# Kernel tuning notes

Measured on AMD Instinct MI355X. Metric: run time of the kernel, lower is better.

Reference implementation:

```python
import jax, jax.numpy as jnp
import numpy as np

EMBED = 1024
HEADS = 16


def setup_inputs() -> dict:
    key = jax.random.key(0)
    ks = jax.random.split(key, 12)
    s = 1.0 / np.sqrt(EMBED)
    return {
        "x": jax.random.normal(ks[0], (1, EMBED, 128, 128), jnp.float32),
        "masks": jax.random.normal(ks[1], (200, 128, 128), jnp.float32),
        "Wq": jax.random.normal(ks[2], (EMBED, EMBED), jnp.float32) * s,
        "bq": jax.random.normal(ks[3], (EMBED,), jnp.float32) * 0.02,
        "Wk": jax.random.normal(ks[4], (EMBED, EMBED), jnp.float32) * s,
        "bk": jax.random.normal(ks[5], (EMBED,), jnp.float32) * 0.02,
        "Wv": jax.random.normal(ks[6], (EMBED, EMBED), jnp.float32) * s,
        "bv": jax.random.normal(ks[7], (EMBED,), jnp.float32) * 0.02,
        "Wc": jax.random.normal(ks[8], (EMBED, EMBED), jnp.float32) * s,
        "bc": jax.random.normal(ks[9], (EMBED,), jnp.float32) * 0.02,
    }


def reference(x, masks, Wq, bq, Wk, bk, Wv, bv, Wc, bc):
    # x: [1, C, H, W], masks: [Q, H, W]  (way4 branch, batch must be 1)
    N, C, H, W = x.shape
    Q = masks.shape[0]
    HW = H * W
    nh = HEADS
    hd = C // nh

    xs = x.reshape(C, HW).T                      # [HW, C] pixel tokens
    m = jax.nn.sigmoid(masks).reshape(Q, HW).T   # [HW, Q]

    # mask-weighted mean pooling (avoid materializing [HW, Q, C])
    w = jnp.sum(m, axis=0)                       # [Q]
    mean = jnp.einsum('lq,lc->qc', m, xs) / (w[:, None] + 0.001)  # [Q, C]

    seq = jnp.concatenate([mean, xs], axis=0)    # [L, C], L = Q + HW
    L = Q + HW

    q = (mean @ Wq.T + bq).reshape(Q, nh, hd) * (hd ** -0.5)
    k = (seq @ Wk.T + bk).reshape(L, nh, hd)
    v = (seq @ Wv.T + bv).reshape(L, nh, hd)

    # bool attn mask [Q, L]: True = disallowed
    qq = ~jnp.eye(Q, dtype=bool)                 # only self among pooled queries
    qp = (m.T <= 0.9)                            # pixels with sigmoid <= 0.9 masked
    attn_mask = jnp.concatenate([qq, qp], axis=1)  # [Q, L]

    scores = jnp.einsum('qhd,lhd->hql', q, k)    # [nh, Q, L]
    scores = jnp.where(attn_mask[None], -jnp.inf, scores)
    probs = jax.nn.softmax(scores, axis=-1)
    ctx = jnp.einsum('hql,lhd->qhd', probs, v).reshape(Q, C)
    out = ctx @ Wc.T + bc                        # [Q, out_dim]
    return out.reshape(Q, 1, -1)                 # match torch [Q, batch=1, out_dim]
```

## Files before the change

kernel.cpp:

```cpp
#include <hip/hip_runtime.h>
#include <math.h>

#define HW_  16384
#define Q_   200
#define C_   1024
#define L_   16584
#define NH_  16
#define HD_  64
#define CAP  512
#define KSPLIT 8
#define KCH  (HW_ / KSPLIT)
#define ASPLIT 4
#define SK   4

typedef __attribute__((ext_vector_type(8))) __bf16 bf16x8;
typedef __attribute__((ext_vector_type(8))) unsigned short u16x8;
typedef __attribute__((ext_vector_type(4))) unsigned short u16x4;
typedef __attribute__((ext_vector_type(4))) float f32x4;

__device__ inline unsigned short f2bf(float f) {
  unsigned int u = __float_as_uint(f);
  u += 0x7fff + ((u >> 16) & 1);
  return (unsigned short)(u >> 16);
}
__device__ inline float bf2f(unsigned short u) {
  return __uint_as_float((unsigned int)u << 16);
}


__global__ __launch_bounds__(256) void k_sig_compact(const float* __restrict__ masks,
                                                     unsigned short* __restrict__ msigbf,
                                                     float* __restrict__ w,
                                                     int* __restrict__ cnt,
                                                     int* __restrict__ idxg) {
  int q = blockIdx.x;
  int tid = threadIdx.x;
  unsigned short* obf = msigbf + (size_t)q * HW_;
  if (q >= Q_) {
    u16x4 z = {0, 0, 0, 0};
    for (int i = tid; i < HW_ / 4; i += 256) *(u16x4*)&obf[i * 4] = z;
    return;
  }
  const float* mrow = masks + (size_t)q * HW_;
  const int base = tid * 64;
  unsigned long long bits = 0;
  float s = 0.f;
  #pragma unroll
  for (int j4 = 0; j4 < 16; j4++) {
    float4 v = *(const float4*)&mrow[base + j4 * 4];
    float sg0 = 1.f / (1.f + expf(-v.x));
    float sg1 = 1.f / (1.f + expf(-v.y));
    float sg2 = 1.f / (1.f + expf(-v.z));
    float sg3 = 1.f / (1.f + expf(-v.w));
    u16x4 o = {f2bf(sg0), f2bf(sg1), f2bf(sg2), f2bf(sg3)};
    *(u16x4*)&obf[base + j4 * 4] = o;
    s += sg0 + sg1 + sg2 + sg3;
    if (sg0 > 0.9f) bits |= 1ull << (j4 * 4 + 0);
    if (sg1 > 0.9f) bits |= 1ull << (j4 * 4 + 1);
    if (sg2 > 0.9f) bits |= 1ull << (j4 * 4 + 2);
    if (sg3 > 0.9f) bits |= 1ull << (j4 * 4 + 3);
  }
  int my = __popcll(bits);

  __shared__ float red[256];
  __shared__ int sc[256];
  red[tid] = s;
  sc[tid] = my;
  __syncthreads();
  for (int off = 128; off > 0; off >>= 1) {
    if (tid < off) red[tid] += red[tid + off];
    __syncthreads();
  }
  if (tid == 0) w[q] = red[0];
  for (int off = 1; off < 256; off <<= 1) {
    int v = sc[tid];
    int add = (tid >= off) ? sc[tid - off] : 0;
    __syncthreads();
    sc[tid] = v + add;
    __syncthreads();
  }
  int excl = sc[tid] - my;
  int total = sc[255];
  int* orow = idxg + (size_t)q * CAP;
  int off = 1 + excl;
  for (int j = 0; j < 64; j++) {
    if ((bits >> j) & 1ull) {
      if (off < CAP) orow[off] = Q_ + base + j;
      off++;
    }
  }
  if (tid == 0) {
    orow[0] = q;
    int c = 1 + total;
    cnt[q] = c < CAP ? c : CAP;
  }
}

__global__ __launch_bounds__(256) void k_xcast(const float* __restrict__ x,
                                               unsigned short* __restrict__ xbf,
                                               unsigned short* __restrict__ seqbf) {
  __shared__ float t[32][33];
  int l0 = blockIdx.x * 32, c0 = blockIdx.y * 32;
  int tx = threadIdx.x, ty = threadIdx.y;
  #pragma unroll
  for (int i = 0; i < 32; i += 8) {
    float v = x[(size_t)(c0 + ty + i) * HW_ + l0 + tx];
    t[ty + i][tx] = v;
    xbf[(size_t)(c0 + ty + i) * HW_ + l0 + tx] = f2bf(v);
  }
  __syncthreads();
  #pragma unroll
  for (int i = 0; i < 32; i += 8)
    seqbf[(size_t)(Q_ + l0 + ty + i) * C_ + c0 + tx] = f2bf(t[tx][ty + i]);
}

__global__ __launch_bounds__(256) void k_cast4(const float* __restrict__ s0,
                                               const float* __restrict__ s1,
                                               const float* __restrict__ s2,
                                               const float* __restrict__ s3,
                                               unsigned short* __restrict__ d0,
                                               unsigned short* __restrict__ d1,
                                               unsigned short* __restrict__ d2,
                                               unsigned short* __restrict__ d3) {
  const float* src = (blockIdx.y == 0) ? s0 : (blockIdx.y == 1) ? s1
                     : (blockIdx.y == 2) ? s2 : s3;
  unsigned short* dst = (blockIdx.y == 0) ? d0 : (blockIdx.y == 1) ? d1
                        : (blockIdx.y == 2) ? d2 : d3;
  int i = (blockIdx.x * 256 + threadIdx.x) * 4;
  float4 v = *(const float4*)&src[i];
  u16x4 o = {f2bf(v.x), f2bf(v.y), f2bf(v.z), f2bf(v.w)};
  *(u16x4*)&dst[i] = o;
}

#define GBM 128
#define GBN 128
#define GBK 32

__global__ __launch_bounds__(512) void k_gemm_kv(const unsigned short* __restrict__ A,
                                                 const unsigned short* __restrict__ Bk,
                                                 const unsigned short* __restrict__ Bv,
                                                 const float* __restrict__ bk,
                                                 const float* __restrict__ bv,
                                                 unsigned short* __restrict__ Ko,
                                                 unsigned short* __restrict__ Vo,
                                                 int M, int K) {
  __shared__ __attribute__((aligned(16))) unsigned short smem[3][3 * GBM * GBK];
  int w = blockIdx.x;
  int nbm = gridDim.x >> 3;
  int t = (w >> 3) + (w & 7) * nbm;
  int bm = (t >> 3) * GBM;
  int bn = (t & 7) * GBN;
  int tid = threadIdx.x;
  int wid = tid >> 6, lane = tid & 63;
  int w2 = wid & 3;
  int wr = w2 >> 1, wc = w2 & 1;
  int fq = lane >> 4, fr = lane & 15;
  int srow = lane >> 2;
  int scol = (((lane & 3) ^ ((lane >> 3) & 3)) * 8);
  int sslot = (fq ^ ((fr >> 1) & 3)) * 8;
  int boff = (wid < 4) ? GBM * GBK : 2 * GBM * GBK;

  auto stage = [&](int buf, int k0) {
    #pragma unroll
    for (int i = 0; i < 3; i++) {
      int ci = wid * 3 + i;
      const unsigned short* src;
      if (ci < 8) {
        int gA = bm + ci * 16 + srow; if (gA > M - 1) gA = M - 1;
        src = A + (size_t)gA * K + k0 + scol;
      } else if (ci < 16) {
        src = Bk + (size_t)(bn + (ci - 8) * 16 + srow) * K + k0 + scol;
      } else {
        src = Bv + (size_t)(bn + (ci - 16) * 16 + srow) * K + k0 + scol;
      }
      __builtin_amdgcn_global_load_lds(
          (const __attribute__((address_space(1))) void*)src,
          (__attribute__((address_space(3))) void*)((char*)&smem[buf][0] + ci * 1024),
          16, 0, 0);
    }
  };

  f32x4 acc[4][4] = {};
  const int NT = K / GBK;
  stage(0, 0);
  stage(1, GBK);
  for (int it = 0; it < NT; it++) {
    int cur = it % 3;
    asm volatile("" ::: "memory");
    __builtin_amdgcn_s_barrier();
    asm volatile("" ::: "memory");
    if (it + 2 < NT) {
      stage((it + 2) % 3, (it + 2) * GBK);
      asm volatile("s_waitcnt vmcnt(6)" ::: "memory");
    } else if (it + 1 < NT) {
      asm volatile("s_waitcnt vmcnt(3)" ::: "memory");
    } else {
      asm volatile("s_waitcnt vmcnt(0)" ::: "memory");
    }
    const unsigned short (*As)[GBK]  = (const unsigned short (*)[GBK])(&smem[cur][0]);
    const unsigned short (*Bts)[GBK] = (const unsigned short (*)[GBK])(&smem[cur][0] + boff);
    bf16x8 af[4], bfr[4];
    #pragma unroll
    for (int mi = 0; mi < 4; mi++)
      af[mi] = *(const bf16x8*)&As[wr * 64 + mi * 16 + fr][sslot];
    #pragma unroll
    for (int ni = 0; ni < 4; ni++)
      bfr[ni] = *(const bf16x8*)&Bts[wc * 64 + ni * 16 + fr][sslot];
    __builtin_amdgcn_s_setprio(1);
    #pragma unroll
    for (int mi = 0; mi < 4; mi++)
      #pragma unroll
      for (int ni = 0; ni < 4; ni++)
        acc[mi][ni] = __builtin_amdgcn_mfma_f32_16x16x32_bf16(bfr[ni], af[mi], acc[mi][ni], 0, 0, 0);
    __builtin_amdgcn_s_setprio(0);
  }
  const float* bias = (wid < 4) ? bk : bv;
  unsigned short* Cout = (wid < 4) ? Ko : Vo;
  #pragma unroll
  for (int mi = 0; mi < 4; mi++) {
    int m = bm + wr * 64 + mi * 16 + fr;
    if (m >= M) continue;
    #pragma unroll
    for (int ni = 0; ni < 4; ni++) {
      int n0 = bn + wc * 64 + ni * 16 + fq * 4;
      float4 b4 = *(const float4*)&bias[n0];
      u16x4 o = {f2bf(acc[mi][ni][0] + b4.x), f2bf(acc[mi][ni][1] + b4.y),
                 f2bf(acc[mi][ni][2] + b4.z), f2bf(acc[mi][ni][3] + b4.w)};
      *(u16x4*)&Cout[(size_t)m * C_ + n0] = o;
    }
  }
}

__global__ __launch_bounds__(256) void k_gemm_meank(const unsigned short* __restrict__ A,
                                                    const unsigned short* __restrict__ B,
                                                    float* __restrict__ partial) {
  __shared__ __attribute__((aligned(16))) unsigned short As[2][GBM][GBK];
  __shared__ __attribute__((aligned(16))) unsigned short Bs[2][GBN][GBK];
  int bm = blockIdx.y * GBM, bn = blockIdx.x * GBN;
  int kc = blockIdx.z;
  int tid = threadIdx.x;
  int wid = tid >> 6, lane = tid & 63;
  int wr = wid >> 1, wc = wid & 1;
  int fq = lane >> 4, fr = lane & 15;
  int srow = lane >> 2;
  int scol = (((lane & 3) ^ ((lane >> 3) & 3)) * 8);
  int sslot = (fq ^ ((fr >> 1) & 3)) * 8;

  auto stage = [&](int buf, int k0) {
    #pragma unroll
    for (int i = 0; i < 2; i++) {
      int r = wid * 32 + i * 16 + srow;
      __builtin_amdgcn_global_load_lds(
          (const __attribute__((address_space(1))) void*)(A + (size_t)(bm + r) * HW_ + k0 + scol),
          (__attribute__((address_space(3))) void*)((char*)&As[buf][0][0] + (wid * 2 + i) * 1024),
          16, 0, 0);
      __builtin_amdgcn_global_load_lds(
          (const __attribute__((address_space(1))) void*)(B + (size_t)(bn + r) * HW_ + k0 + scol),
          (__attribute__((address_space(3))) void*)((char*)&Bs[buf][0][0] + (wid * 2 + i) * 1024),
          16, 0, 0);
    }
  };

  f32x4 acc[4][4] = {};
  int kbeg = kc * KCH;
  const int NT = KCH / GBK;
  stage(0, kbeg);
  __syncthreads();
  int cur = 0;
  for (int it = 0; it < NT; it++) {
    if (it + 1 < NT) stage(cur ^ 1, kbeg + (it + 1) * GBK);
    bf16x8 af[4], bfr[4];
    #pragma unroll
    for (int mi = 0; mi < 4; mi++)
      af[mi] = *(const bf16x8*)&As[cur][wr * 64 + mi * 16 + fr][sslot];
    #pragma unroll
    for (int ni = 0; ni < 4; ni++)
      bfr[ni] = *(const bf16x8*)&Bs[cur][wc * 64 + ni * 16 + fr][sslot];
    #pragma unroll
    for (int mi = 0; mi < 4; mi++)
      #pragma unroll
      for (int ni = 0; ni < 4; ni++)
        acc[mi][ni] = __builtin_amdgcn_mfma_f32_16x16x32_bf16(bfr[ni], af[mi], acc[mi][ni], 0, 0, 0);
    __syncthreads();
    cur ^= 1;
  }
  #pragma unroll
  for (int mi = 0; mi < 4; mi++) {
    int m = bm + wr * 64 + mi * 16 + fr;
    #pragma unroll
    for (int ni = 0; ni < 4; ni++) {
      int n0 = bn + wc * 64 + ni * 16 + fq * 4;
      *(f32x4*)&partial[((size_t)kc * 256 + m) * C_ + n0] = acc[mi][ni];
    }
  }
}

__global__ __launch_bounds__(256) void k_mean_reduce(const float* __restrict__ partial,
                                                     const float* __restrict__ w,
                                                     unsigned short* __restrict__ seqbf) {
  int m = blockIdx.x;
  float rs = 1.f / (w[m] + 0.001f);
  for (int n = threadIdx.x; n < C_; n += 256) {
    float s = 0.f;
    #pragma unroll
    for (int kc = 0; kc < KSPLIT; kc++)
      s += partial[((size_t)kc * 256 + m) * C_ + n];
    seqbf[(size_t)m * C_ + n] = f2bf(s * rs);
  }
}

__global__ __launch_bounds__(256) void k_gemm_splitk_bf(const unsigned short* __restrict__ A,
                                                        const unsigned short* __restrict__ B,
                                                        float* __restrict__ partial,
                                                        int M, int K) {
  __shared__ __attribute__((aligned(16))) unsigned short As[2][GBM][GBK];
  __shared__ __attribute__((aligned(16))) unsigned short Bs[2][GBN][GBK];
  int bm = blockIdx.y * GBM, bn = blockIdx.x * GBN;
  int kc = blockIdx.z;
  int kchunk = K / SK;
  int tid = threadIdx.x;
  int wid = tid >> 6, lane = tid & 63;
  int wr = wid >> 1, wc = wid & 1;
  int fq = lane >> 4, fr = lane & 15;
  int srow = lane >> 2;
  int scol = (((lane & 3) ^ ((lane >> 3) & 3)) * 8);
  int sslot = (fq ^ ((fr >> 1) & 3)) * 8;

  auto stage = [&](int buf, int k0) {
    #pragma unroll
    for (int i = 0; i < 2; i++) {
      int r = wid * 32 + i * 16 + srow;
      int gA = bm + r; if (gA > M - 1) gA = M - 1;
      __builtin_amdgcn_global_load_lds(
          (const __attribute__((address_space(1))) void*)(A + (size_t)gA * K + k0 + scol),
          (__attribute__((address_space(3))) void*)((char*)&As[buf][0][0] + (wid * 2 + i) * 1024),
          16, 0, 0);
      __builtin_amdgcn_global_load_lds(
          (const __attribute__((address_space(1))) void*)(B + (size_t)(bn + r) * K + k0 + scol),
          (__attribute__((address_space(3))) void*)((char*)&Bs[buf][0][0] + (wid * 2 + i) * 1024),
          16, 0, 0);
    }
  };

  f32x4 acc[4][4] = {};
  int kbeg = kc * kchunk;
  const int NT = kchunk / GBK;
  stage(0, kbeg);
  __syncthreads();
  int cur = 0;
  for (int it = 0; it < NT; it++) {
    if (it + 1 < NT) stage(cur ^ 1, kbeg + (it + 1) * GBK);
    bf16x8 af[4], bfr[4];
    #pragma unroll
    for (int mi = 0; mi < 4; mi++)
      af[mi] = *(const bf16x8*)&As[cur][wr * 64 + mi * 16 + fr][sslot];
    #pragma unroll
    for (int ni = 0; ni < 4; ni++)
      bfr[ni] = *(const bf16x8*)&Bs[cur][wc * 64 + ni * 16 + fr][sslot];
    #pragma unroll
    for (int mi = 0; mi < 4; mi++)
      #pragma unroll
      for (int ni = 0; ni < 4; ni++)
        acc[mi][ni] = __builtin_amdgcn_mfma_f32_16x16x32_bf16(bfr[ni], af[mi], acc[mi][ni], 0, 0, 0);
    __syncthreads();
    cur ^= 1;
  }
  #pragma unroll
  for (int mi = 0; mi < 4; mi++) {
    int m = bm + wr * 64 + mi * 16 + fr;
    #pragma unroll
    for (int ni = 0; ni < 4; ni++) {
      int n0 = bn + wc * 64 + ni * 16 + fq * 4;
      *(f32x4*)&partial[((size_t)kc * 256 + m) * C_ + n0] = acc[mi][ni];
    }
  }
}

__global__ __launch_bounds__(256) void k_splitk_reduce(const float* __restrict__ partial,
                                                       const float* __restrict__ bias,
                                                       float* __restrict__ outf) {
  int m = blockIdx.x;
  for (int n = threadIdx.x; n < C_; n += 256) {
    float s = 0.f;
    #pragma unroll
    for (int kc = 0; kc < SK; kc++)
      s += partial[((size_t)kc * 256 + m) * C_ + n];
    outf[(size_t)m * C_ + n] = s + bias[n];
  }
}

__global__ __launch_bounds__(256) void k_attn_split(const float* __restrict__ qpart,
                                                    const float* __restrict__ bq,
                                                    const unsigned short* __restrict__ kb,
                                                    const unsigned short* __restrict__ vb,
                                                    const int* __restrict__ cnt_g,
                                                    const int* __restrict__ idxg,
                                                    float* __restrict__ pmax,
                                                    float* __restrict__ psum,
                                                    float* __restrict__ pacc) {
  int q = blockIdx.x, h = blockIdx.y, sp = blockIdx.z;
  int tid = threadIdx.x;
  int lane = tid & 63, wid = tid >> 6;

  __shared__ float qs[64];
  __shared__ float sc[CAP / ASPLIT];
  __shared__ int   ls[CAP / ASPLIT];
  __shared__ float wred[4];
  __shared__ float accb[4][64];

  int cnt = cnt_g[q];
  int cq = (cnt + ASPLIT - 1) / ASPLIT;
  int beg = sp * cq;
  int end = beg + cq; if (end > cnt) end = cnt;
  int ns = end - beg; if (ns < 0) ns = 0;

  if (tid < 64) {
    float s = bq[h * HD_ + tid];
    #pragma unroll
    for (int kc = 0; kc < SK; kc++)
      s += qpart[((size_t)kc * 256 + q) * C_ + h * HD_ + tid];
    qs[tid] = s * 0.125f;
  }
  __syncthreads();

  for (int i0 = 0; i0 < ns; i0 += 64) {
    int i = i0 + (tid >> 2);
    if (i < ns) {
      int sub = tid & 3;
      int l = idxg[(size_t)q * CAP + beg + i];
      const u16x8* kr = (const u16x8*)(kb + (size_t)l * C_ + h * HD_ + sub * 16);
      u16x8 kv0 = kr[0], kv1 = kr[1];
      float s = 0.f;
      #pragma unroll
      for (int e = 0; e < 8; e++) s = fmaf(qs[sub * 16 + e], bf2f(kv0[e]), s);
      #pragma unroll
      for (int e = 0; e < 8; e++) s = fmaf(qs[sub * 16 + 8 + e], bf2f(kv1[e]), s);
      s += __shfl_xor(s, 1);
      s += __shfl_xor(s, 2);
      if (sub == 0) { sc[i] = s; ls[i] = l; }
    }
  }
  __syncthreads();

  float lm = (tid < ns) ? sc[tid] : -INFINITY;
  #pragma unroll
  for (int off = 32; off; off >>= 1) lm = fmaxf(lm, __shfl_xor(lm, off));
  if (lane == 0) wred[wid] = lm;
  __syncthreads();
  float m4 = fmaxf(fmaxf(wred[0], wred[1]), fmaxf(wred[2], wred[3]));

  float e = 0.f;
  if (tid < ns) {
    e = expf(sc[tid] - m4);
    sc[tid] = e;
  }
  float lsum = e;
  #pragma unroll
  for (int off = 32; off; off >>= 1) lsum += __shfl_xor(lsum, off);
  __syncthreads();
  if (lane == 0) wred[wid] = lsum;
  __syncthreads();
  float S4 = wred[0] + wred[1] + wred[2] + wred[3];

  float acc = 0.f;
  for (int j = wid; j < ns; j += 4)
    acc = fmaf(sc[j], bf2f(vb[(size_t)ls[j] * C_ + h * HD_ + lane]), acc);
  accb[wid][lane] = acc;
  __syncthreads();

  int pidx = (q * NH_ + h) * ASPLIT + sp;
  if (tid < 64)
    pacc[(size_t)pidx * 64 + tid] =
        accb[0][tid] + accb[1][tid] + accb[2][tid] + accb[3][tid];
  if (tid == 0) {
    pmax[pidx] = (ns > 0) ? m4 : -INFINITY;
    psum[pidx] = S4;
  }
}

__global__ __launch_bounds__(64) void k_attn_merge(const float* __restrict__ pmax,
                                                   const float* __restrict__ psum,
                                                   const float* __restrict__ pacc,
                                                   unsigned short* __restrict__ ctxbf) {
  int q = blockIdx.x, h = blockIdx.y;
  int d = threadIdx.x;
  int base = (q * NH_ + h) * ASPLIT;
  float M = -INFINITY;
  #pragma unroll
  for (int s = 0; s < ASPLIT; s++) M = fmaxf(M, pmax[base + s]);
  float S = 0.f, a = 0.f;
  #pragma unroll
  for (int s = 0; s < ASPLIT; s++) {
    float wgt = expf(pmax[base + s] - M);
    S += psum[base + s] * wgt;
    a += pacc[(size_t)(base + s) * 64 + d] * wgt;
  }
  ctxbf[(size_t)q * C_ + h * HD_ + d] = f2bf(a / S);
}

extern "C" void kernel_launch(void* const* d_in, const int* in_sizes, int n_in,
                              void* d_out, int out_size, void* d_ws, size_t ws_size,
                              hipStream_t stream) {
  const float* x     = (const float*)d_in[0];
  const float* masks = (const float*)d_in[1];
  const float* Wq    = (const float*)d_in[2];
  const float* bq    = (const float*)d_in[3];
  const float* Wk    = (const float*)d_in[4];
  const float* bk    = (const float*)d_in[5];
  const float* Wv    = (const float*)d_in[6];
  const float* bv    = (const float*)d_in[7];
  const float* Wc    = (const float*)d_in[8];
  const float* bc    = (const float*)d_in[9];
  float* out = (float*)d_out;

  char* p = (char*)d_ws;
  auto alloc = [&](size_t bytes) {
    char* r = p;
    p += (bytes + 255) & ~(size_t)255;
    return r;
  };
  float* w       = (float*)alloc(1024);
  float* partial = (float*)alloc((size_t)KSPLIT * 256 * C_ * 4);
  float* qpart   = (float*)alloc((size_t)SK * 256 * C_ * 4);
  int*   cnt     = (int*)alloc(1024);
  int*   idxg    = (int*)alloc((size_t)Q_ * CAP * 4);
  float* pmax    = (float*)alloc((size_t)Q_ * NH_ * ASPLIT * 4);
  float* psum    = (float*)alloc((size_t)Q_ * NH_ * ASPLIT * 4);
  float* pacc    = (float*)alloc((size_t)Q_ * NH_ * ASPLIT * 64 * 4);
  unsigned short* msigbf = (unsigned short*)alloc((size_t)256 * HW_ * 2);
  unsigned short* xbf    = (unsigned short*)alloc((size_t)C_ * HW_ * 2);
  unsigned short* seqbf  = (unsigned short*)alloc((size_t)L_ * C_ * 2);
  unsigned short* wkbf   = (unsigned short*)alloc((size_t)C_ * C_ * 2);
  unsigned short* wvbf   = (unsigned short*)alloc((size_t)C_ * C_ * 2);
  unsigned short* wqbf   = (unsigned short*)alloc((size_t)C_ * C_ * 2);
  unsigned short* wcbf   = (unsigned short*)alloc((size_t)C_ * C_ * 2);
  unsigned short* ctxbf  = (unsigned short*)alloc((size_t)256 * C_ * 2);
  unsigned short* kbuf   = (unsigned short*)alloc((size_t)L_ * C_ * 2);
  unsigned short* vbuf   = (unsigned short*)alloc((size_t)L_ * C_ * 2);

  k_sig_compact<<<256, 256, 0, stream>>>(masks, msigbf, w, cnt, idxg);
  k_xcast<<<dim3(HW_ / 32, C_ / 32), dim3(32, 8), 0, stream>>>(x, xbf, seqbf);
  k_cast4<<<dim3(C_ * C_ / 1024, 4), 256, 0, stream>>>(Wk, Wv, Wq, Wc,
                                                       wkbf, wvbf, wqbf, wcbf);
  k_gemm_meank<<<dim3(C_ / GBN, 2, KSPLIT), 256, 0, stream>>>(msigbf, xbf, partial);
  k_mean_reduce<<<Q_, 256, 0, stream>>>(partial, w, seqbf);
  k_gemm_splitk_bf<<<dim3(C_ / GBN, 2, SK), 256, 0, stream>>>(seqbf, wqbf, qpart, Q_, C_);
  k_gemm_kv<<<8 * ((L_ + GBM - 1) / GBM), 512, 0, stream>>>(
      seqbf, wkbf, wvbf, bk, bv, kbuf, vbuf, L_, C_);
  k_attn_split<<<dim3(Q_, NH_, ASPLIT), 256, 0, stream>>>(
      qpart, bq, kbuf, vbuf, cnt, idxg, pmax, psum, pacc);
  k_attn_merge<<<dim3(Q_, NH_), 64, 0, stream>>>(pmax, psum, pacc, ctxbf);
  k_gemm_splitk_bf<<<dim3(C_ / GBN, 2, SK), 256, 0, stream>>>(ctxbf, wcbf, partial, Q_, C_);
  k_splitk_reduce<<<Q_, 256, 0, stream>>>(partial, bc, out);
}
```

Measured before the change: 267.2 us.

## Restructure K/V projection GEMM into 256x128 tiles with concatenated weights and quarter pipelining

Replaces the fused K/V GEMM with a kernel that treats Wk and Wv as one concatenated 2048-row weight matrix, using 256x128 output tiles with BK=64 and double-buffered LDS. The loads are split into A and B halves interleaved with four MFMA quarter-steps, with separate waitcnt/barrier points so global-to-LDS copies overlap compute. The goal is higher arithmetic intensity per tile and better latency hiding in the dominant GEMM. In exchange LDS use and register pressure go up, and the fixed swizzle adds complexity. The hardcoded grid mapping (130 M-tiles) ties the kernel to this problem size.

```diff
diff --git a/kernel.cpp b/kernel.cpp
--- a/kernel.cpp
+++ b/kernel.cpp
@@ -26,7 +26,6 @@
 __device__ inline float bf2f(unsigned short u) {
   return __uint_as_float((unsigned int)u << 16);
 }
-
 
 __global__ __launch_bounds__(256) void k_sig_compact(const float* __restrict__ masks,
                                                      unsigned short* __restrict__ msigbf,
@@ -136,97 +135,138 @@
 #define GBN 128
 #define GBK 32
 
-__global__ __launch_bounds__(512) void k_gemm_kv(const unsigned short* __restrict__ A,
-                                                 const unsigned short* __restrict__ Bk,
-                                                 const unsigned short* __restrict__ Bv,
-                                                 const float* __restrict__ bk,
-                                                 const float* __restrict__ bv,
-                                                 unsigned short* __restrict__ Ko,
-                                                 unsigned short* __restrict__ Vo,
-                                                 int M, int K) {
-  __shared__ __attribute__((aligned(16))) unsigned short smem[3][3 * GBM * GBK];
-  int w = blockIdx.x;
-  int nbm = gridDim.x >> 3;
-  int t = (w >> 3) + (w & 7) * nbm;
-  int bm = (t >> 3) * GBM;
-  int bn = (t & 7) * GBN;
+__global__ __launch_bounds__(512) void k_gemm_kv8(const unsigned short* __restrict__ A,
+                                                  const unsigned short* __restrict__ Wkv,
+                                                  const float* __restrict__ bk,
+                                                  const float* __restrict__ bv,
+                                                  unsigned short* __restrict__ Ko,
+                                                  unsigned short* __restrict__ Vo,
+                                                  int M) {
+  __shared__ __attribute__((aligned(16))) unsigned short lds[2][24576];
+  const int K = 1024;
+  int wg = blockIdx.x;
+  int t = (wg >> 3) + (wg & 7) * 130;
+  int bm = (t >> 4) * 256;
+  int bn = (t & 15) * 128;
   int tid = threadIdx.x;
   int wid = tid >> 6, lane = tid & 63;
-  int w2 = wid & 3;
-  int wr = w2 >> 1, wc = w2 & 1;
+  int wm = wid >> 1;
+  int wn = wid & 1;
   int fq = lane >> 4, fr = lane & 15;
-  int srow = lane >> 2;
-  int scol = (((lane & 3) ^ ((lane >> 3) & 3)) * 8);
-  int sslot = (fq ^ ((fr >> 1) & 3)) * 8;
-  int boff = (wid < 4) ? GBM * GBK : 2 * GBM * GBK;
-
-  auto stage = [&](int buf, int k0) {
-    #pragma unroll
-    for (int i = 0; i < 3; i++) {
-      int ci = wid * 3 + i;
-      const unsigned short* src;
-      if (ci < 8) {
-        int gA = bm + ci * 16 + srow; if (gA > M - 1) gA = M - 1;
-        src = A + (size_t)gA * K + k0 + scol;
-      } else if (ci < 16) {
-        src = Bk + (size_t)(bn + (ci - 8) * 16 + srow) * K + k0 + scol;
-      } else {
-        src = Bv + (size_t)(bn + (ci - 16) * 16 + srow) * K + k0 + scol;
+  int frs = (fr >> 1) & 7;
+
+  auto stageA = [&](int nb, int mh, int k0) {
+    #pragma unroll
+    for (int i = 0; i < 2; i++) {
+      int j = wid * 2 + i;
+      int row0 = (j >> 2) * 64 + mh * 32 + (j & 3) * 8;
+      int r = row0 + (lane >> 3);
+      int g = bm + r; if (g > M - 1) g = M - 1;
+      int swz = (r >> 1) & 7;
+      int col = k0 + (((lane & 7) ^ swz) << 3);
+      __builtin_amdgcn_global_load_lds(
+          (const __attribute__((address_space(1))) void*)(A + (size_t)g * K + col),
+          (__attribute__((address_space(3))) void*)((char*)&lds[nb][0] + row0 * 128),
+          16, 0, 0);
+    }
+  };
+  auto stageB = [&](int nb, int nh, int k0) {
+    int j = wid;
+    int row0 = (j >> 2) * 64 + nh * 32 + (j & 3) * 8;
+    int r = row0 + (lane >> 3);
+    int g = bn + r;
+    int swz = (r >> 1) & 7;
+    int col = k0 + (((lane & 7) ^ swz) << 3);
+    __builtin_amdgcn_global_load_lds(
+        (const __attribute__((address_space(1))) void*)(Wkv + (size_t)g * K + col),
+        (__attribute__((address_space(3))) void*)((char*)&lds[nb][16384] + row0 * 128),
+        16, 0, 0);
+  };
+
+  f32x4 acc[4][4] = {};
+  bf16x8 Aa[2][2], B0[2][2], B1[2][2];
+
+  auto rdA = [&](int buf, int mh) {
+    #pragma unroll
+    for (int ml = 0; ml < 2; ml++)
+      #pragma unroll
+      for (int ks = 0; ks < 2; ks++) {
+        int row = wm * 64 + (mh * 2 + ml) * 16 + fr;
+        Aa[ml][ks] = *(const bf16x8*)&lds[buf][(row << 6) + ((((ks << 2) + fq) ^ frs) << 3)];
       }
-      __builtin_amdgcn_global_load_lds(
-          (const __attribute__((address_space(1))) void*)src,
-          (__attribute__((address_space(3))) void*)((char*)&smem[buf][0] + ci * 1024),
-          16, 0, 0);
-    }
-  };
-
-  f32x4 acc[4][4] = {};
-  const int NT = K / GBK;
-  stage(0, 0);
-  stage(1, GBK);
-  for (int it = 0; it < NT; it++) {
-    int cur = it % 3;
-    asm volatile("" ::: "memory");
+  };
+  auto rdB = [&](bf16x8 (&Bb)[2][2], int buf, int nh) {
+    #pragma unroll
+    for (int nl = 0; nl < 2; nl++)
+      #pragma unroll
+      for (int ks = 0; ks < 2; ks++) {
+        int row = wn * 64 + (nh * 2 + nl) * 16 + fr;
+        Bb[nl][ks] = *(const bf16x8*)&lds[buf][16384 + (row << 6) + ((((ks << 2) + fq) ^ frs) << 3)];
+      }
+  };
+  auto mm = [&](bf16x8 (&Bb)[2][2], int mh, int nh) {
+    __builtin_amdgcn_s_setprio(1);
+    #pragma unroll
+    for (int ml = 0; ml < 2; ml++)
+      #pragma unroll
+      for (int nl = 0; nl < 2; nl++)
+        #pragma unroll
+        for (int ks = 0; ks < 2; ks++)
+          acc[mh * 2 + ml][nh * 2 + nl] = __builtin_amdgcn_mfma_f32_16x16x32_bf16(
+              Bb[nl][ks], Aa[ml][ks], acc[mh * 2 + ml][nh * 2 + nl], 0, 0, 0);
+    __builtin_amdgcn_s_setprio(0);
+  };
+
+  stageA(0, 0, 0);
+  stageB(0, 0, 0);
+  stageB(0, 1, 0);
+  stageA(0, 1, 0);
+
+  const int NT = 16;
+  for (int kt = 0; kt < NT; kt++) {
+    int buf = kt & 1, nb = buf ^ 1;
+    int k0n = (kt + 1) * 64;
+    bool stg = (kt + 1 < NT);
+    if (stg) { stageA(nb, 0, k0n); asm volatile("s_waitcnt vmcnt(5)" ::: "memory"); }
+    else     {                     asm volatile("s_waitcnt vmcnt(3)" ::: "memory"); }
     __builtin_amdgcn_s_barrier();
     asm volatile("" ::: "memory");
-    if (it + 2 < NT) {
-      stage((it + 2) % 3, (it + 2) * GBK);
-      asm volatile("s_waitcnt vmcnt(6)" ::: "memory");
-    } else if (it + 1 < NT) {
-      asm volatile("s_waitcnt vmcnt(3)" ::: "memory");
-    } else {
-      asm volatile("s_waitcnt vmcnt(0)" ::: "memory");
-    }
-    const unsigned short (*As)[GBK]  = (const unsigned short (*)[GBK])(&smem[cur][0]);
-    const unsigned short (*Bts)[GBK] = (const unsigned short (*)[GBK])(&smem[cur][0] + boff);
-    bf16x8 af[4], bfr[4];
-    #pragma unroll
-    for (int mi = 0; mi < 4; mi++)
-      af[mi] = *(const bf16x8*)&As[wr * 64 + mi * 16 + fr][sslot];
-    #pragma unroll
-    for (int ni = 0; ni < 4; ni++)
-      bfr[ni] = *(const bf16x8*)&Bts[wc * 64 + ni * 16 + fr][sslot];
-    __builtin_amdgcn_s_setprio(1);
-    #pragma unroll
-    for (int mi = 0; mi < 4; mi++)
-      #pragma unroll
-      for (int ni = 0; ni < 4; ni++)
-        acc[mi][ni] = __builtin_amdgcn_mfma_f32_16x16x32_bf16(bfr[ni], af[mi], acc[mi][ni], 0, 0, 0);
-    __builtin_amdgcn_s_setprio(0);
-  }
-  const float* bias = (wid < 4) ? bk : bv;
-  unsigned short* Cout = (wid < 4) ? Ko : Vo;
-  #pragma unroll
-  for (int mi = 0; mi < 4; mi++) {
-    int m = bm + wr * 64 + mi * 16 + fr;
-    if (m >= M) continue;
-    #pragma unroll
-    for (int ni = 0; ni < 4; ni++) {
-      int n0 = bn + wc * 64 + ni * 16 + fq * 4;
+    rdA(buf, 0);
+    rdB(B0, buf, 0);
+    mm(B0, 0, 0);
+    if (stg) { stageB(nb, 0, k0n); asm volatile("s_waitcnt vmcnt(5)" ::: "memory"); }
+    else     {                     asm volatile("s_waitcnt vmcnt(2)" ::: "memory"); }
+    __builtin_amdgcn_s_barrier();
+    asm volatile("" ::: "memory");
+    rdB(B1, buf, 1);
+    mm(B1, 0, 1);
+    if (stg) { stageB(nb, 1, k0n); asm volatile("s_waitcnt vmcnt(4)" ::: "memory"); }
+    else     {                     asm volatile("s_waitcnt vmcnt(0)" ::: "memory"); }
+    __builtin_amdgcn_s_barrier();
+    asm volatile("" ::: "memory");
+    rdA(buf, 1);
+    mm(B0, 1, 0);
+    if (stg) { stageA(nb, 1, k0n); asm volatile("s_waitcnt vmcnt(6)" ::: "memory"); }
+    else     {                     asm volatile("s_waitcnt vmcnt(0)" ::: "memory"); }
+    __builtin_amdgcn_s_barrier();
+    asm volatile("" ::: "memory");
+    mm(B1, 1, 1);
+  }
+
+  const float* bias = (bn < 1024) ? bk : bv;
+  unsigned short* Cout = (bn < 1024) ? Ko : Vo;
+  int bnc = bn & 1023;
+  #pragma unroll
+  for (int m = 0; m < 4; m++) {
+    int mg = bm + wm * 64 + m * 16 + fr;
+    if (mg >= M) continue;
+    #pragma unroll
+    for (int n = 0; n < 4; n++) {
+      int n0 = bnc + wn * 64 + n * 16 + fq * 4;
       float4 b4 = *(const float4*)&bias[n0];
-      u16x4 o = {f2bf(acc[mi][ni][0] + b4.x), f2bf(acc[mi][ni][1] + b4.y),
-                 f2bf(acc[mi][ni][2] + b4.z), f2bf(acc[mi][ni][3] + b4.w)};
-      *(u16x4*)&Cout[(size_t)m * C_ + n0] = o;
+      u16x4 o = {f2bf(acc[m][n][0] + b4.x), f2bf(acc[m][n][1] + b4.y),
+                 f2bf(acc[m][n][2] + b4.z), f2bf(acc[m][n][3] + b4.w)};
+      *(u16x4*)&Cout[(size_t)mg * C_ + n0] = o;
     }
   }
 }
@@ -530,8 +570,7 @@
   unsigned short* msigbf = (unsigned short*)alloc((size_t)256 * HW_ * 2);
   unsigned short* xbf    = (unsigned short*)alloc((size_t)C_ * HW_ * 2);
   unsigned short* seqbf  = (unsigned short*)alloc((size_t)L_ * C_ * 2);
-  unsigned short* wkbf   = (unsigned short*)alloc((size_t)C_ * C_ * 2);
-  unsigned short* wvbf   = (unsigned short*)alloc((size_t)C_ * C_ * 2);
+  unsigned short* wkvbf  = (unsigned short*)alloc((size_t)2048 * C_ * 2);
   unsigned short* wqbf   = (unsigned short*)alloc((size_t)C_ * C_ * 2);
   unsigned short* wcbf   = (unsigned short*)alloc((size_t)C_ * C_ * 2);
   unsigned short* ctxbf  = (unsigned short*)alloc((size_t)256 * C_ * 2);
@@ -540,13 +579,12 @@
 
   k_sig_compact<<<256, 256, 0, stream>>>(masks, msigbf, w, cnt, idxg);
   k_xcast<<<dim3(HW_ / 32, C_ / 32), dim3(32, 8), 0, stream>>>(x, xbf, seqbf);
-  k_cast4<<<dim3(C_ * C_ / 1024, 4), 256, 0, stream>>>(Wk, Wv, Wq, Wc,
-                                                       wkbf, wvbf, wqbf, wcbf);
+  k_cast4<<<dim3(C_ * C_ / 1024, 4), 256, 0, stream>>>(
+      Wk, Wv, Wq, Wc, wkvbf, wkvbf + (size_t)1024 * C_, wqbf, wcbf);
   k_gemm_meank<<<dim3(C_ / GBN, 2, KSPLIT), 256, 0, stream>>>(msigbf, xbf, partial);
   k_mean_reduce<<<Q_, 256, 0, stream>>>(partial, w, seqbf);
   k_gemm_splitk_bf<<<dim3(C_ / GBN, 2, SK), 256, 0, stream>>>(seqbf, wqbf, qpart, Q_, C_);
-  k_gemm_kv<<<8 * ((L_ + GBM - 1) / GBM), 512, 0, stream>>>(
-      seqbf, wkbf, wvbf, bk, bv, kbuf, vbuf, L_, C_);
+  k_gemm_kv8<<<8 * 130, 512, 0, stream>>>(seqbf, wkvbf, bk, bv, kbuf, vbuf, L_);
   k_attn_split<<<dim3(Q_, NH_, ASPLIT), 256, 0, stream>>>(
       qpart, bq, kbuf, vbuf, cnt, idxg, pmax, psum, pacc);
   k_attn_merge<<<dim3(Q_, NH_), 64, 0, stream>>>(pmax, psum, pacc, ctxbf);
```

Result: no change. 271.5 us (+1.6%).
